# Kernel optimization log

Hardware: AMD Instinct MI355X
Metric: run time of the kernel (lower is better)

## Reference

```python
import jax, jax.numpy as jnp
import numpy as np

ENC, PRED, H, V, DMAX = 1024, 640, 640, 1024, 4
B, T, U = 4, 256, 64


def setup_inputs() -> dict:
    key = jax.random.key(0)
    ks = jax.random.split(key, 10)
    s = lambda d: 1.0 / np.sqrt(d)
    return {
        "encoder_out": jax.random.normal(ks[0], (B, T, ENC), jnp.float32),
        "predictor_out": jax.random.normal(ks[1], (B, U, PRED), jnp.float32),
        "W_enc": jax.random.uniform(ks[2], (H, ENC), jnp.float32, -s(ENC), s(ENC)),
        "b_enc": jax.random.uniform(ks[3], (H,), jnp.float32, -s(ENC), s(ENC)),
        "W_pred": jax.random.uniform(ks[4], (H, PRED), jnp.float32, -s(PRED), s(PRED)),
        "b_pred": jax.random.uniform(ks[5], (H,), jnp.float32, -s(PRED), s(PRED)),
        "W_out": jax.random.uniform(ks[6], (V, H), jnp.float32, -s(H), s(H)),
        "b_out": jax.random.uniform(ks[7], (V,), jnp.float32, -s(H), s(H)),
        "W_dur": jax.random.uniform(ks[8], (DMAX + 1, H), jnp.float32, -s(H), s(H)),
        "b_dur": jax.random.uniform(ks[9], (DMAX + 1,), jnp.float32, -s(H), s(H)),
    }


def reference(encoder_out, predictor_out, W_enc, b_enc, W_pred, b_pred,
              W_out, b_out, W_dur, b_dur):
    # Project encoder [B,T,H] and predictor [B,U,H]
    enc = jnp.einsum('bte,he->bth', encoder_out, W_enc) + b_enc
    pred = jnp.einsum('bup,hp->buh', predictor_out, W_pred) + b_pred
    # Broadcast-add -> [B,T,U,H], tanh
    joint = jnp.tanh(enc[:, :, None, :] + pred[:, None, :, :])
    # Dual heads
    logits = jnp.einsum('btuh,vh->btuv', joint, W_out) + b_out        # [B,T,U,V]
    durations = jnp.einsum('btuh,dh->btud', joint, W_dur) + b_dur     # [B,T,U,DMAX+1]
    return (logits, durations)
```

## Files before the change

### kernel.cpp

```cpp
#include <hip/hip_runtime.h>

typedef unsigned short u16;
typedef unsigned int u32;

typedef __bf16 bf16x8 __attribute__((ext_vector_type(8)));
typedef float f32x4 __attribute__((ext_vector_type(4)));

union FragI { int4 i; bf16x8 b; };
union FragU { bf16x8 b; u16 u[8]; };

__device__ __forceinline__ u16 f2bf(float x) {
  u32 u = __float_as_uint(x);
  u32 r = (u + 0x7fffu + ((u >> 16) & 1u)) >> 16;
  return (u16)r;
}

__device__ __forceinline__ float tanh_fast(float x) {
  float e = __expf(2.0f * x);
  return 1.0f - __fdividef(2.0f, e + 1.0f);
}

__device__ __forceinline__ bf16x8 load_cvt8(const float* __restrict__ p) {
  float4 f0 = *(const float4*)p;
  float4 f1 = *(const float4*)(p + 4);
  FragU t;
  t.u[0] = f2bf(f0.x); t.u[1] = f2bf(f0.y); t.u[2] = f2bf(f0.z); t.u[3] = f2bf(f0.w);
  t.u[4] = f2bf(f1.x); t.u[5] = f2bf(f1.y); t.u[6] = f2bf(f1.z); t.u[7] = f2bf(f1.w);
  return t.b;
}

#define GLDS(gptr, lptr) \
  __builtin_amdgcn_global_load_lds((const __attribute__((address_space(1))) u32*)(gptr), \
                                   (__attribute__((address_space(3))) u32*)(lptr), 16, 0, 0)

__global__ __launch_bounds__(256) void conv_v4(const float* __restrict__ in,
                                               u16* __restrict__ out, int n4) {
  int i = blockIdx.x * 256 + threadIdx.x;
  if (i >= n4) return;
  float4 f = ((const float4*)in)[i];
  union { u16 u[4]; int2 v; } o;
  o.u[0] = f2bf(f.x); o.u[1] = f2bf(f.y); o.u[2] = f2bf(f.z); o.u[3] = f2bf(f.w);
  ((int2*)out)[i] = o.v;
}

__global__ __launch_bounds__(256) void proj_gemm(const float* __restrict__ A,
                                                 const float* __restrict__ Bw,
                                                 const float* __restrict__ bias,
                                                 float* __restrict__ C,
                                                 int M, int N, int K) {
  int tid = threadIdx.x;
  int lane = tid & 63, wid = tid >> 6;
  int m0 = blockIdx.x * 64, n0 = blockIdx.y * 64;
  int kper = K >> 2;
  int kbase = wid * kper;
  int ksteps = kper >> 5;
  int r16 = lane & 15, khi = (lane >> 4) * 8;

  f32x4 z = {0.f, 0.f, 0.f, 0.f};
  f32x4 acc[4][4];
  for (int i = 0; i < 4; ++i)
    for (int j = 0; j < 4; ++j) acc[i][j] = z;

  for (int ks = 0; ks < ksteps; ++ks) {
    int k = kbase + ks * 32 + khi;
    bf16x8 af[4], bf[4];
#pragma unroll
    for (int fm = 0; fm < 4; ++fm)
      af[fm] = load_cvt8(A + (size_t)(m0 + fm * 16 + r16) * K + k);
#pragma unroll
    for (int fn = 0; fn < 4; ++fn)
      bf[fn] = load_cvt8(Bw + (size_t)(n0 + fn * 16 + r16) * K + k);
#pragma unroll
    for (int fm = 0; fm < 4; ++fm)
#pragma unroll
      for (int fn = 0; fn < 4; ++fn)
        acc[fm][fn] = __builtin_amdgcn_mfma_f32_16x16x32_bf16(af[fm], bf[fn], acc[fm][fn], 0, 0, 0);
  }

  __shared__ float red[4][64][64];
#pragma unroll
  for (int fm = 0; fm < 4; ++fm)
#pragma unroll
    for (int fn = 0; fn < 4; ++fn)
#pragma unroll
      for (int i = 0; i < 4; ++i)
        red[wid][fm * 16 + (lane >> 4) * 4 + i][fn * 16 + r16] = acc[fm][fn][i];
  __syncthreads();
  for (int idx = tid; idx < 4096; idx += 256) {
    int r = idx >> 6, c = idx & 63;
    float s = red[0][r][c] + red[1][r][c] + red[2][r][c] + red[3][r][c] + bias[n0 + c];
    C[(size_t)(m0 + r) * N + n0 + c] = s;
  }
}

__global__ __launch_bounds__(256) void joint_tanh(const float* __restrict__ enc,
                                                  const float* __restrict__ pred,
                                                  u16* __restrict__ J) {
  const int total = 65536 * 80;
  for (int c = blockIdx.x * 256 + threadIdx.x; c < total; c += gridDim.x * 256) {
    int m = c / 80;
    int j = c - m * 80;
    int bt = m >> 6;
    int uu = m & 63;
    int b = bt >> 8;
    const float* ep = enc + bt * 640 + j * 8;
    const float* pp = pred + (b * 64 + uu) * 640 + j * 8;
    float4 e0 = *(const float4*)ep;
    float4 e1 = *(const float4*)(ep + 4);
    float4 p0 = *(const float4*)pp;
    float4 p1 = *(const float4*)(pp + 4);
    union { u16 u[8]; int4 v; } o;
    o.u[0] = f2bf(tanh_fast(e0.x + p0.x));
    o.u[1] = f2bf(tanh_fast(e0.y + p0.y));
    o.u[2] = f2bf(tanh_fast(e0.z + p0.z));
    o.u[3] = f2bf(tanh_fast(e0.w + p0.w));
    o.u[4] = f2bf(tanh_fast(e1.x + p1.x));
    o.u[5] = f2bf(tanh_fast(e1.y + p1.y));
    o.u[6] = f2bf(tanh_fast(e1.z + p1.z));
    o.u[7] = f2bf(tanh_fast(e1.w + p1.w));
    *(int4*)(J + (size_t)c * 8) = o.v;
  }
}

#define LOGITS_N 67108864

__device__ __forceinline__ void stage256(const u16* __restrict__ g, u16* l,
                                         int wid, int lane) {
  int rl = wid * 8 + (lane >> 3);
  int cl = ((lane & 7) ^ (lane >> 3)) * 8;
  const u16* gp = g + (size_t)rl * 640 + cl;
  u16* lp = l + wid * 512;
#pragma unroll
  for (int j = 0; j < 4; ++j)
    GLDS(gp + (size_t)j * 64 * 640, lp + j * 4096);
}

__global__ __launch_bounds__(512, 2) void main_gemm(const u16* __restrict__ J,
                                                    const u16* __restrict__ Wo,
                                                    const float* __restrict__ W_dur,
                                                    const float* __restrict__ b_out,
                                                    const float* __restrict__ b_dur,
                                                    float* __restrict__ out) {
  __shared__ __align__(16) u16 As[2][16384];
  __shared__ __align__(16) u16 Bs[2][16384];
  __shared__ __align__(16) u16 Ws[10240];
  int tid = threadIdx.x;
  int lane = tid & 63, wid = tid >> 6;
  int bid = blockIdx.x;
  int swz = (bid & 7) * 128 + (bid >> 3);
  int bn = swz & 3, bm = swz >> 2;
  int m0 = bm * 256, n0 = bn * 256;
  int wr = wid >> 2, wc = wid & 3;
  int r16 = lane & 15, khi = (lane >> 4) * 8;
  int xorv = (r16 & 7) << 3;
  bool do_dur = (bn == 0);

  if (do_dur) {
    for (int i = tid; i < 10240; i += 512)
      Ws[i] = (i < 3200) ? f2bf(W_dur[i]) : (u16)0;
  }

  f32x4 z = {0.f, 0.f, 0.f, 0.f};
  f32x4 acc[8][4];
#pragma unroll
  for (int i = 0; i < 8; ++i)
#pragma unroll
    for (int j = 0; j < 4; ++j) acc[i][j] = z;
  f32x4 dacc[8];
#pragma unroll
  for (int i = 0; i < 8; ++i) dacc[i] = z;

  const u16* Jb = J + (size_t)m0 * 640;
  const u16* Wb = Wo + (size_t)n0 * 640;
  stage256(Jb + 0, As[0], wid, lane);
  stage256(Wb + 0, Bs[0], wid, lane);
  stage256(Jb + 64, As[1], wid, lane);
  stage256(Wb + 64, Bs[1], wid, lane);
  asm volatile("s_waitcnt lgkmcnt(0)" ::: "memory");

#pragma unroll
  for (int t = 0; t < 10; ++t) {
    const int p = t & 1;
    if (t < 9) {
      asm volatile("s_waitcnt vmcnt(8)" ::: "memory");
    } else {
      asm volatile("s_waitcnt vmcnt(0)" ::: "memory");
    }
    __builtin_amdgcn_sched_barrier(0);
    __builtin_amdgcn_s_barrier();
    __builtin_amdgcn_sched_barrier(0);
    const u16* Ab = As[p];
    const u16* Bb = Bs[p];
#pragma unroll
    for (int ks = 0; ks < 2; ++ks) {
      int cks = (ks * 32 + khi) ^ xorv;
      FragI bfr[4], af[8], wd;
#pragma unroll
      for (int fn = 0; fn < 4; ++fn)
        bfr[fn].i = *(const int4*)(Bb + (wc * 64 + fn * 16 + r16) * 64 + cks);
#pragma unroll
      for (int fm = 0; fm < 8; ++fm)
        af[fm].i = *(const int4*)(Ab + (wr * 128 + fm * 16 + r16) * 64 + cks);
      if (do_dur)
        wd.i = *(const int4*)(Ws + r16 * 640 + t * 64 + ks * 32 + khi);
      __builtin_amdgcn_s_setprio(1);
#pragma unroll
      for (int fm = 0; fm < 8; ++fm) {
#pragma unroll
        for (int fn = 0; fn < 4; ++fn)
          acc[fm][fn] = __builtin_amdgcn_mfma_f32_16x16x32_bf16(af[fm].b, bfr[fn].b, acc[fm][fn], 0, 0, 0);
        if (do_dur)
          dacc[fm] = __builtin_amdgcn_mfma_f32_16x16x32_bf16(af[fm].b, wd.b, dacc[fm], 0, 0, 0);
      }
      __builtin_amdgcn_s_setprio(0);
    }
    if (t < 9) {
      __builtin_amdgcn_sched_barrier(0);
      asm volatile("s_waitcnt lgkmcnt(0)" ::: "memory");
      __builtin_amdgcn_s_barrier();
      __builtin_amdgcn_sched_barrier(0);
      if (t + 2 < 10) {
        stage256(Jb + (t + 2) * 64, As[p], wid, lane);
        stage256(Wb + (t + 2) * 64, Bs[p], wid, lane);
      }
    }
  }

  int rb = m0 + wr * 128 + (lane >> 4) * 4;
  int cb = n0 + wc * 64 + r16;
#pragma unroll
  for (int fn = 0; fn < 4; ++fn) {
    int col = cb + fn * 16;
    float bo = b_out[col];
#pragma unroll
    for (int fm = 0; fm < 8; ++fm) {
      int row = rb + fm * 16;
#pragma unroll
      for (int i = 0; i < 4; ++i)
        out[(size_t)(row + i) * 1024 + col] = acc[fm][fn][i] + bo;
    }
  }
  if (do_dur && r16 < 5) {
    float bd = b_dur[r16];
#pragma unroll
    for (int fm = 0; fm < 8; ++fm) {
      int row = rb + fm * 16;
#pragma unroll
      for (int i = 0; i < 4; ++i)
        out[LOGITS_N + (size_t)(row + i) * 5 + r16] = dacc[fm][i] + bd;
    }
  }
}

extern "C" void kernel_launch(void* const* d_in, const int* in_sizes, int n_in,
                              void* d_out, int out_size, void* d_ws, size_t ws_size,
                              hipStream_t stream) {
  const float* encoder   = (const float*)d_in[0];
  const float* predictor = (const float*)d_in[1];
  const float* W_enc = (const float*)d_in[2];
  const float* b_enc = (const float*)d_in[3];
  const float* W_pred = (const float*)d_in[4];
  const float* b_pred = (const float*)d_in[5];
  const float* W_out = (const float*)d_in[6];
  const float* b_out = (const float*)d_in[7];
  const float* W_dur = (const float*)d_in[8];
  const float* b_dur = (const float*)d_in[9];
  float* out = (float*)d_out;

  char* ws = (char*)d_ws;
  u16* Jbuf    = (u16*)(ws);
  u16* WoutB   = (u16*)(ws + 83886080);
  float* encP  = (float*)(ws + 85196800);
  float* predP = (float*)(ws + 87818240);

  conv_v4<<<640, 256, 0, stream>>>(W_out, WoutB, 163840);
  proj_gemm<<<dim3(16, 10), 256, 0, stream>>>(encoder, W_enc, b_enc, encP, 1024, 640, 1024);
  proj_gemm<<<dim3(4, 10), 256, 0, stream>>>(predictor, W_pred, b_pred, predP, 256, 640, 640);
  joint_tanh<<<2048, 256, 0, stream>>>(encP, predP, Jbuf);
  main_gemm<<<1024, 512, 0, stream>>>(Jbuf, WoutB, W_dur, b_out, b_dur, out);
}
```

Baseline: 201.8 us.

## Interleave staging loads with MFMA phases and restrict duration head to one wave column

```diff
diff --git a/kernel.cpp b/kernel.cpp
--- a/kernel.cpp
+++ b/kernel.cpp
@@ -123,16 +123,16 @@
 }
 
 #define LOGITS_N 67108864
-
-__device__ __forceinline__ void stage256(const u16* __restrict__ g, u16* l,
-                                         int wid, int lane) {
+#define WS_LD 648
+
+__device__ __forceinline__ void stage_half(const u16* __restrict__ g, u16* l,
+                                           int wid, int lane) {
   int rl = wid * 8 + (lane >> 3);
   int cl = ((lane & 7) ^ (lane >> 3)) * 8;
   const u16* gp = g + (size_t)rl * 640 + cl;
   u16* lp = l + wid * 512;
-#pragma unroll
-  for (int j = 0; j < 4; ++j)
-    GLDS(gp + (size_t)j * 64 * 640, lp + j * 4096);
+  GLDS(gp, lp);
+  GLDS(gp + (size_t)64 * 640, lp + 4096);
 }
 
 __global__ __launch_bounds__(512, 2) void main_gemm(const u16* __restrict__ J,
@@ -143,7 +143,8 @@
                                                     float* __restrict__ out) {
   __shared__ __align__(16) u16 As[2][16384];
   __shared__ __align__(16) u16 Bs[2][16384];
-  __shared__ __align__(16) u16 Ws[10240];
+  __shared__ __align__(16) u16 Ws[16 * WS_LD];
+
   int tid = threadIdx.x;
   int lane = tid & 63, wid = tid >> 6;
   int bid = blockIdx.x;
@@ -151,14 +152,25 @@
   int bn = swz & 3, bm = swz >> 2;
   int m0 = bm * 256, n0 = bn * 256;
   int wr = wid >> 2, wc = wid & 3;
-  int r16 = lane & 15, khi = (lane >> 4) * 8;
+  int r16 = lane & 15, khi8 = (lane >> 4) * 8;
   int xorv = (r16 & 7) << 3;
-  bool do_dur = (bn == 0);
-
-  if (do_dur) {
-    for (int i = tid; i < 10240; i += 512)
-      Ws[i] = (i < 3200) ? f2bf(W_dur[i]) : (u16)0;
-  }
+  bool dur_blk = (bn == 0);
+  bool do_dur = dur_blk && (wc == 0);
+
+  if (dur_blk) {
+    for (int i = tid; i < 16 * WS_LD; i += 512) {
+      int r = i / WS_LD, c = i - r * WS_LD;
+      Ws[i] = (r < 5 && c < 640) ? f2bf(W_dur[r * 640 + c]) : (u16)0;
+    }
+  }
+  const u16* JA = J + (size_t)m0 * 640;
+  const u16* WB = Wo + (size_t)n0 * 640;
+  stage_half(JA, As[0], wid, lane);
+  stage_half(JA + (size_t)128 * 640, As[0] + 8192, wid, lane);
+  stage_half(WB, Bs[0], wid, lane);
+  stage_half(WB + (size_t)128 * 640, Bs[0] + 8192, wid, lane);
+  asm volatile("s_waitcnt lgkmcnt(0)" ::: "memory");
+  __builtin_amdgcn_sched_barrier(0);
 
   f32x4 z = {0.f, 0.f, 0.f, 0.f};
   f32x4 acc[8][4];
@@ -170,59 +182,79 @@
 #pragma unroll
   for (int i = 0; i < 8; ++i) dacc[i] = z;
 
-  const u16* Jb = J + (size_t)m0 * 640;
-  const u16* Wb = Wo + (size_t)n0 * 640;
-  stage256(Jb + 0, As[0], wid, lane);
-  stage256(Wb + 0, Bs[0], wid, lane);
-  stage256(Jb + 64, As[1], wid, lane);
-  stage256(Wb + 64, Bs[1], wid, lane);
-  asm volatile("s_waitcnt lgkmcnt(0)" ::: "memory");
-
-#pragma unroll
-  for (int t = 0; t < 10; ++t) {
-    const int p = t & 1;
-    if (t < 9) {
-      asm volatile("s_waitcnt vmcnt(8)" ::: "memory");
-    } else {
-      asm volatile("s_waitcnt vmcnt(0)" ::: "memory");
-    }
-    __builtin_amdgcn_sched_barrier(0);
-    __builtin_amdgcn_s_barrier();
-    __builtin_amdgcn_sched_barrier(0);
-    const u16* Ab = As[p];
-    const u16* Bb = Bs[p];
-#pragma unroll
-    for (int ks = 0; ks < 2; ++ks) {
-      int cks = (ks * 32 + khi) ^ xorv;
-      FragI bfr[4], af[8], wd;
-#pragma unroll
-      for (int fn = 0; fn < 4; ++fn)
-        bfr[fn].i = *(const int4*)(Bb + (wc * 64 + fn * 16 + r16) * 64 + cks);
-#pragma unroll
-      for (int fm = 0; fm < 8; ++fm)
-        af[fm].i = *(const int4*)(Ab + (wr * 128 + fm * 16 + r16) * 64 + cks);
-      if (do_dur)
-        wd.i = *(const int4*)(Ws + r16 * 640 + t * 64 + ks * 32 + khi);
+  FragI bfr[4][2], wd[2];
+
+  for (int it = 0; it < 5; ++it) {
+    int t0 = 2 * it;
+#pragma unroll
+    for (int p = 0; p < 8; ++p) {
+      const int q = p & 3;
+      const int b = p >> 2;
+      const int tc = t0 + b;
+
+      if (q == 0) {
+        asm volatile("s_waitcnt vmcnt(0)" ::: "memory");
+        __builtin_amdgcn_sched_barrier(0);
+        __builtin_amdgcn_s_barrier();
+        __builtin_amdgcn_sched_barrier(0);
+      }
+
+      const u16* Ab = As[b];
+      const u16* Bb = Bs[b];
+      FragI aq[2][2];
+#pragma unroll
+      for (int m = 0; m < 2; ++m)
+#pragma unroll
+        for (int ks = 0; ks < 2; ++ks)
+          aq[m][ks].i = *(const int4*)(Ab + (wr * 128 + q * 32 + m * 16 + r16) * 64 +
+                                       ((ks * 32 + khi8) ^ xorv));
+      if (q == 0) {
+#pragma unroll
+        for (int fn = 0; fn < 4; ++fn)
+#pragma unroll
+          for (int ks = 0; ks < 2; ++ks)
+            bfr[fn][ks].i = *(const int4*)(Bb + (wc * 64 + fn * 16 + r16) * 64 +
+                                           ((ks * 32 + khi8) ^ xorv));
+        if (do_dur) {
+#pragma unroll
+          for (int ks = 0; ks < 2; ++ks)
+            wd[ks].i = *(const int4*)(Ws + r16 * WS_LD + tc * 64 + ks * 32 + khi8);
+        }
+      }
+
+      if (b == 0 || it < 4) {
+        const int ts = t0 + 1 + b;
+        u16* dA = As[1 - b];
+        u16* dB = Bs[1 - b];
+        if (p == 0 || p == 4) stage_half(JA + (size_t)ts * 64, dA, wid, lane);
+        if (p == 1 || p == 5) stage_half(JA + (size_t)(128 * 640) + ts * 64, dA + 8192, wid, lane);
+        if (p == 2 || p == 6) stage_half(WB + (size_t)ts * 64, dB, wid, lane);
+        if (p == 3 || p == 7) stage_half(WB + (size_t)(128 * 640) + ts * 64, dB + 8192, wid, lane);
+      }
+
+      if (q != 0) {
+        __builtin_amdgcn_s_barrier();
+      }
+      asm volatile("s_waitcnt lgkmcnt(0)" ::: "memory");
+      __builtin_amdgcn_sched_barrier(0);
+
       __builtin_amdgcn_s_setprio(1);
 #pragma unroll
-      for (int fm = 0; fm < 8; ++fm) {
-#pragma unroll
-        for (int fn = 0; fn < 4; ++fn)
-          acc[fm][fn] = __builtin_amdgcn_mfma_f32_16x16x32_bf16(af[fm].b, bfr[fn].b, acc[fm][fn], 0, 0, 0);
-        if (do_dur)
-          dacc[fm] = __builtin_amdgcn_mfma_f32_16x16x32_bf16(af[fm].b, wd.b, dacc[fm], 0, 0, 0);
+      for (int m = 0; m < 2; ++m) {
+#pragma unroll
+        for (int ks = 0; ks < 2; ++ks) {
+#pragma unroll
+          for (int fn = 0; fn < 4; ++fn)
+            acc[q * 2 + m][fn] = __builtin_amdgcn_mfma_f32_16x16x32_bf16(
+                aq[m][ks].b, bfr[fn][ks].b, acc[q * 2 + m][fn], 0, 0, 0);
+          if (do_dur)
+            dacc[q * 2 + m] = __builtin_amdgcn_mfma_f32_16x16x32_bf16(
+                aq[m][ks].b, wd[ks].b, dacc[q * 2 + m], 0, 0, 0);
+        }
       }
       __builtin_amdgcn_s_setprio(0);
-    }
-    if (t < 9) {
       __builtin_amdgcn_sched_barrier(0);
-      asm volatile("s_waitcnt lgkmcnt(0)" ::: "memory");
       __builtin_amdgcn_s_barrier();
-      __builtin_amdgcn_sched_barrier(0);
-      if (t + 2 < 10) {
-        stage256(Jb + (t + 2) * 64, As[p], wid, lane);
-        stage256(Wb + (t + 2) * 64, Bs[p], wid, lane);
-      }
     }
   }
 
```

Result: slower. 209.7 us (+3.9%).
